# Optimization experiments

Measured on AMD Instinct MI355X. Metric: run time of the kernel, lower is better.

Reference implementation:

```python
import jax, jax.numpy as jnp
import numpy as np

B, S, D, H, F = 4, 1024, 1024, 16, 4096
DH = D // H
EPS = 1e-5


def _ln(x, g, b):
    mu = jnp.mean(x, axis=-1, keepdims=True)
    var = jnp.mean((x - mu) ** 2, axis=-1, keepdims=True)
    return (x - mu) * jax.lax.rsqrt(var + EPS) * g + b


def _mha(q_in, k_in, v_in, mask, wq, bq, wk, bk, wv, bv, wo, bo):
    b, sq, d = q_in.shape
    sk = k_in.shape[1]
    Q = (q_in @ wq + bq).reshape(b, sq, H, DH).transpose(0, 2, 1, 3)  # [B,H,Sq,dh]
    K = (k_in @ wk + bk).reshape(b, sk, H, DH).transpose(0, 2, 1, 3)
    V = (v_in @ wv + bv).reshape(b, sk, H, DH).transpose(0, 2, 1, 3)
    scores = jnp.einsum('bhqd,bhkd->bhqk', Q, K) / jnp.sqrt(jnp.asarray(DH, Q.dtype))
    if mask is not None:
        scores = jnp.where(mask[:, None] == 0, jnp.asarray(-1e9, scores.dtype), scores)
    w = jax.nn.softmax(scores, axis=-1)
    ctx = jnp.einsum('bhqk,bhkd->bhqd', w, V).transpose(0, 2, 1, 3).reshape(b, sq, d)
    return ctx @ wo + bo


def setup_inputs() -> dict:
    key = jax.random.key(0)
    ks = jax.random.split(key, 20)
    s = 0.02
    inp = {
        'x': jax.random.normal(ks[0], (B, S, D), jnp.float32),
        'src_x': jax.random.normal(ks[1], (B, S, D), jnp.float32),
        # causal self-attention mask (1 = keep), cross mask all ones
        'mask': jnp.broadcast_to(jnp.tril(jnp.ones((S, S), jnp.int32)), (B, S, S)),
        'src_mask': jnp.ones((B, S, S), jnp.int32),
        'ln1_g': jnp.ones((D,), jnp.float32), 'ln1_b': jnp.zeros((D,), jnp.float32),
        'ln2_g': jnp.ones((D,), jnp.float32), 'ln2_b': jnp.zeros((D,), jnp.float32),
        'ln3_g': jnp.ones((D,), jnp.float32), 'ln3_b': jnp.zeros((D,), jnp.float32),
    }
    names = ['sa_wq', 'sa_wk', 'sa_wv', 'sa_wo', 'ca_wq', 'ca_wk', 'ca_wv', 'ca_wo']
    for i, n in enumerate(names):
        inp[n] = jax.random.normal(ks[2 + i], (D, D), jnp.float32) * s
        inp[n.replace('w', 'b')] = jnp.zeros((D,), jnp.float32)
    inp['ff_w1'] = jax.random.normal(ks[10], (D, F), jnp.float32) * s
    inp['ff_b1'] = jnp.zeros((F,), jnp.float32)
    inp['ff_w2'] = jax.random.normal(ks[11], (F, D), jnp.float32) * s
    inp['ff_b2'] = jnp.zeros((D,), jnp.float32)
    return inp


def reference(x, mask, src_x, src_mask,
              ln1_g, ln1_b, ln2_g, ln2_b, ln3_g, ln3_b,
              sa_wq, sa_bq, sa_wk, sa_bk, sa_wv, sa_bv, sa_wo, sa_bo,
              ca_wq, ca_bq, ca_wk, ca_bk, ca_wv, ca_bv, ca_wo, ca_bo,
              ff_w1, ff_b1, ff_w2, ff_b2):
    # pre-layer-norm decoder layer (dropout = 0 / eval mode)
    h = _ln(x, ln1_g, ln1_b)
    x = x + _mha(h, h, h, mask, sa_wq, sa_bq, sa_wk, sa_bk, sa_wv, sa_bv, sa_wo, sa_bo)
    h = _ln(x, ln2_g, ln2_b)
    x = x + _mha(h, src_x, src_x, src_mask, ca_wq, ca_bq, ca_wk, ca_bk, ca_wv, ca_bv, ca_wo, ca_bo)
    h = _ln(x, ln3_g, ln3_b)
    x = x + (jax.nn.relu(h @ ff_w1 + ff_b1) @ ff_w2 + ff_b2)
    return x
```

## Files before the change

### kernel.cpp

```cpp
#include <hip/hip_runtime.h>
#include <hip/hip_bf16.h>

#define B_ 4
#define S_ 1024
#define D_ 1024
#define H_ 16
#define DH_ 64
#define F_ 4096

typedef unsigned short u16;
typedef unsigned int u32;
typedef __attribute__((ext_vector_type(8))) short bf16x8;
typedef __attribute__((ext_vector_type(4))) short bf16x4;
typedef __attribute__((ext_vector_type(4))) float f32x4;

__device__ __forceinline__ float bf2f(u16 u) {
    return __uint_as_float(((u32)u) << 16);
}
__device__ __forceinline__ u16 f2bf(float f) {
    __hip_bfloat16 h = __float2bfloat16(f);
    return *reinterpret_cast<u16*>(&h);
}

typedef __attribute__((address_space(1))) const u32 gu32;
typedef __attribute__((address_space(3))) u32 lu32;
__device__ __forceinline__ void gl_lds16(const void* g, void* l) {
    __builtin_amdgcn_global_load_lds((gu32*)g, (lu32*)l, 16, 0, 0);
}

__global__ __launch_bounds__(256) void cvt1_kernel(const float* __restrict__ s,
                                                   u16* __restrict__ d) {
    int i = (blockIdx.x * 256 + threadIdx.x) * 4;
    float4 v = *(const float4*)(s + i);
    u16 o0 = f2bf(v.x), o1 = f2bf(v.y), o2 = f2bf(v.z), o3 = f2bf(v.w);
    d[i] = o0; d[i+1] = o1; d[i+2] = o2; d[i+3] = o3;
}

__device__ __forceinline__ void trcvt_body(const float* __restrict__ src,
                                           u16* __restrict__ dst, int K, int N,
                                           int n0, int k0) {
    __shared__ u16 tile[64][65];
    int t = threadIdx.x;
    int c = t & 63, r4 = t >> 6;
#pragma unroll
    for (int i = 0; i < 16; i++) {
        int r = i * 4 + r4;
        tile[c][r] = f2bf(src[(size_t)(k0 + r) * N + n0 + c]);
    }
    __syncthreads();
#pragma unroll
    for (int i = 0; i < 16; i++) {
        int rr = i * 4 + r4;
        dst[(size_t)(n0 + rr) * K + k0 + c] = tile[rr][c];
    }
}

__global__ __launch_bounds__(256) void trcvt_kernel(const float* __restrict__ src,
                                                    u16* __restrict__ dst,
                                                    int K, int N) {
    trcvt_body(src, dst, K, N, blockIdx.x * 64, blockIdx.y * 64);
}

struct TP { const float* src[8]; u16* dst[8]; };
__global__ __launch_bounds__(256) void trcvt8_kernel(TP tp) {
    trcvt_body(tp.src[blockIdx.z], tp.dst[blockIdx.z], D_, D_,
               blockIdx.x * 64, blockIdx.y * 64);
}

__global__ __launch_bounds__(256) void mask_reduce_kernel(const int* __restrict__ mask,
                                                          unsigned char* __restrict__ bmask) {
    int t = threadIdx.x;
    int qb = blockIdx.x >> 4, kb = blockIdx.x & 15, b = blockIdx.y;
    bool all1 = true, any1 = false;
#pragma unroll
    for (int i = 0; i < 16; i++) {
        int e = t + i * 256;
        int r = e >> 6, c = e & 63;
        int v = mask[((size_t)(b * S_ + qb * 64 + r)) * S_ + kb * 64 + c];
        all1 = all1 && (v != 0);
        any1 = any1 || (v != 0);
    }
    unsigned long long ba = __ballot(all1), bn = __ballot(any1);
    __shared__ unsigned long long sa[4], sn[4];
    if ((t & 63) == 0) { sa[t >> 6] = ba; sn[t >> 6] = bn; }
    __syncthreads();
    if (t == 0) {
        bool A = ((sa[0] & sa[1] & sa[2] & sa[3]) == ~0ull);
        bool Y = ((sn[0] | sn[1] | sn[2] | sn[3]) != 0ull);
        bmask[b * 256 + blockIdx.x] = A ? 2 : (Y ? 1 : 0);
    }
}

template<bool COPY>
__global__ __launch_bounds__(256) void ln_kernel(const float* __restrict__ xin,
                                                 const float* __restrict__ g,
                                                 const float* __restrict__ bta,
                                                 float* xcur,
                                                 u16* __restrict__ hout) {
    int row = blockIdx.x;
    int t = threadIdx.x;
    size_t base = (size_t)row * D_;
    float v[4];
#pragma unroll
    for (int i = 0; i < 4; i++) v[i] = xin[base + t + i * 256];
    float s  = v[0] + v[1] + v[2] + v[3];
    float s2 = v[0]*v[0] + v[1]*v[1] + v[2]*v[2] + v[3]*v[3];
#pragma unroll
    for (int m = 1; m < 64; m <<= 1) {
        s  += __shfl_xor(s, m);
        s2 += __shfl_xor(s2, m);
    }
    __shared__ float red[8];
    int wave = t >> 6;
    if ((t & 63) == 0) { red[wave*2] = s; red[wave*2+1] = s2; }
    __syncthreads();
    float fs  = red[0] + red[2] + red[4] + red[6];
    float fs2 = red[1] + red[3] + red[5] + red[7];
    float mu  = fs * (1.0f / D_);
    float var = fs2 * (1.0f / D_) - mu * mu;
    float rs  = rsqrtf(var + 1e-5f);
#pragma unroll
    for (int i = 0; i < 4; i++) {
        int c = t + i * 256;
        float x = v[i];
        if (COPY) xcur[base + c] = x;
        hout[base + c] = f2bf((x - mu) * rs * g[c] + bta[c]);
    }
}

struct Bias3 { const float* b0; const float* b1; const float* b2; int n1; int n2; };

__device__ __forceinline__ float bias_at(const Bias3& bs, int c) {
    const float* p; int o;
    if (c < bs.n1)      { p = bs.b0; o = c; }
    else if (c < bs.n2) { p = bs.b1; o = c - bs.n1; }
    else                { p = bs.b2; o = c - bs.n2; }
    return p[o];
}

template<int BM, int BN, int OUT_MODE, bool BIAS_ROW>
__global__ __launch_bounds__(256) void gemm128_kernel(const u16* __restrict__ A,
                                                      const u16* __restrict__ Bt,
                                                      Bias3 bias,
                                                      const float* res,
                                                      void* out,
                                                      int M, int N, int K) {
    constexpr int MT = (BM == 64) ? 4 : (BN == 64 ? 2 : 4);
    constexpr int NT = (BN == 64) ? 4 : (BM == 64 ? 2 : 4);
    __shared__ u16 As[2][BM * 64];
    __shared__ u16 Bs[2][BN * 64];
    int t = threadIdx.x;
    int m0 = blockIdx.y * BM, n0 = blockIdx.x * BN;
    int w = t >> 6, lane = t & 63, quad = lane >> 4, l16 = lane & 15;
    int wm, wn;
    if (BM == 128 && BN == 128) { wm = (w >> 1) * 64; wn = (w & 1) * 64; }
    else if (BN == 64)          { wm = w * 32;        wn = 0; }
    else                        { wm = 0;             wn = w * 32; }

    f32x4 acc[MT][NT] = {};
    int sr = lane >> 3;
    int gc = ((lane & 7) ^ sr) * 8;
    int x7 = l16 & 7;
    const u16* gA = A + (size_t)m0 * K;
    const u16* gB = Bt + (size_t)n0 * K;

    auto stage = [&](int k0, int buf) {
#pragma unroll
        for (int j = w; j < BM / 8; j += 4)
            gl_lds16(gA + (size_t)(j * 8 + sr) * K + k0 + gc, &As[buf][j * 512]);
#pragma unroll
        for (int j = w; j < BN / 8; j += 4)
            gl_lds16(gB + (size_t)(j * 8 + sr) * K + k0 + gc, &Bs[buf][j * 512]);
    };

    stage(0, 0);
    int cur = 0;
    for (int k0 = 0; k0 < K; k0 += 64) {
        __syncthreads();
        if (k0 + 64 < K) stage(k0 + 64, cur ^ 1);

#pragma unroll
        for (int s = 0; s < 2; s++) {
            bf16x8 af[MT], bfr[NT];
            int cp = ((s * 4 + quad) ^ x7) * 8;
#pragma unroll
            for (int mt = 0; mt < MT; mt++)
                af[mt] = *(const bf16x8*)&As[cur][(wm + mt * 16 + l16) * 64 + cp];
#pragma unroll
            for (int nt = 0; nt < NT; nt++)
                bfr[nt] = *(const bf16x8*)&Bs[cur][(wn + nt * 16 + l16) * 64 + cp];
#pragma unroll
            for (int mt = 0; mt < MT; mt++)
#pragma unroll
                for (int nt = 0; nt < NT; nt++)
                    acc[mt][nt] = __builtin_amdgcn_mfma_f32_16x16x32_bf16(af[mt], bfr[nt], acc[mt][nt], 0, 0, 0);
        }
        cur ^= 1;
    }

#pragma unroll
    for (int nt = 0; nt < NT; nt++) {
        int col = n0 + wn + nt * 16 + l16;
        float bc = BIAS_ROW ? 0.f : bias_at(bias, col);
#pragma unroll
        for (int mt = 0; mt < MT; mt++) {
#pragma unroll
            for (int r = 0; r < 4; r++) {
                int row = m0 + wm + mt * 16 + quad * 4 + r;
                float v = acc[mt][nt][r] + (BIAS_ROW ? bias_at(bias, row) : bc);
                if (OUT_MODE == 1) v = fmaxf(v, 0.f);
                if (OUT_MODE == 2) {
                    v += res[(size_t)row * N + col];
                    ((float*)out)[(size_t)row * N + col] = v;
                } else {
                    ((u16*)out)[(size_t)row * N + col] = f2bf(v);
                }
            }
        }
    }
}

__global__ __launch_bounds__(256) void attn_kernel(const u16* __restrict__ Q, int ldq,
                                                   const u16* __restrict__ Kb, int ldk,
                                                   const u16* __restrict__ Vt,
                                                   const int* __restrict__ mask,
                                                   const unsigned char* __restrict__ bmask,
                                                   u16* __restrict__ ctx) {
    __shared__ u16 Ks[2][2][64 * 64];
    __shared__ u16 Vs[2][2][64 * 64];
    int t = threadIdx.x;
    int b = blockIdx.z, hh = blockIdx.y;
    int w = t >> 6, lane = t & 63, quad = lane >> 4, l16 = lane & 15;
    int hoff = hh * DH_;

    int qt[2] = { (int)blockIdx.x, 15 - (int)blockIdx.x };

    bf16x8 ones8;
#pragma unroll
    for (int j = 0; j < 8; j++) ones8[j] = (short)0x3F80;

    bf16x8 qf[2][2];
#pragma unroll
    for (int tt = 0; tt < 2; tt++) {
        int qrow = qt[tt] * 64 + w * 16 + l16;
#pragma unroll
        for (int kk = 0; kk < 2; kk++) {
            bf16x8 v = *(const bf16x8*)(Q + (size_t)(b * S_ + qrow) * ldq + hoff + kk * 32 + quad * 8);
#pragma unroll
            for (int j = 0; j < 8; j++)
                v[j] = (short)f2bf(bf2f((u16)v[j]) * 0.125f);
            qf[tt][kk] = v;
        }
    }

    f32x4 oacc[2][4] = {};
    f32x4 lacc[2] = {};

    unsigned nz[2], mx[2];
#pragma unroll
    for (int tt = 0; tt < 2; tt++) {
        nz[tt] = 0; mx[tt] = 0;
        for (int c = 0; c < 16; c++) {
            int v = bmask ? (int)bmask[(b * 16 + qt[tt]) * 16 + c] : 1;
            if (v)      nz[tt] |= 1u << c;
            if (v == 1) mx[tt] |= 1u << c;
        }
    }
    unsigned nzU = nz[0] | nz[1];
    unsigned remS = 0;
    for (int s = 0; s < 8; s++) if ((nzU >> (2 * s)) & 3u) remS |= 1u << s;

    int sr = lane >> 3;
    int gc = ((lane & 7) ^ sr) * 8;

    auto stage64 = [&](int c, int buf) {
        int k0 = c * 64, c64 = c & 1;
        for (int j = w; j < 8; j += 4) {
            gl_lds16(Kb + (size_t)(b * S_ + k0 + j * 8 + sr) * ldk + hoff + gc, &Ks[buf][c64][j * 512]);
            gl_lds16(Vt + (size_t)(hoff + j * 8 + sr) * (B_ * S_) + b * S_ + k0 + gc, &Vs[buf][c64][j * 512]);
        }
    };
    auto stageS = [&](int s, int buf) {
        if ((nzU >> (2 * s)) & 1u)     stage64(2 * s, buf);
        if ((nzU >> (2 * s + 1)) & 1u) stage64(2 * s + 1, buf);
    };

    int cur = 0;
    int s = remS ? __builtin_ctz(remS) : 8;
    if (s < 8) stageS(s, 0);

    while (s < 8) {
        remS &= remS - 1;
        int ns = remS ? __builtin_ctz(remS) : 8;
        __syncthreads();
        if (ns < 8) stageS(ns, cur ^ 1);

#pragma unroll
        for (int c64 = 0; c64 < 2; c64++) {
            int c = 2 * s + c64;
            if (!((nzU >> c) & 1u)) continue;
            int k0c = c * 64;
            const u16* KsT = &Ks[cur][c64][0];
            const u16* VsT = &Vs[cur][c64][0];

#pragma unroll
            for (int tt = 0; tt < 2; tt++) {
                if (!((nz[tt] >> c) & 1u)) continue;
                bool mixed = (mx[tt] >> c) & 1u;

                float p[4][4];
#pragma unroll
                for (int nt = 0; nt < 4; nt++) {
                    f32x4 sacc = {};
                    int krow = nt * 16 + l16;
#pragma unroll
                    for (int kk = 0; kk < 2; kk++) {
                        int cp = ((kk * 4 + quad) ^ (krow & 7)) * 8;
                        bf16x8 kf = *(const bf16x8*)&KsT[krow * 64 + cp];
                        sacc = __builtin_amdgcn_mfma_f32_16x16x32_bf16(kf, qf[tt][kk], sacc, 0, 0, 0);
                    }
#pragma unroll
                    for (int r = 0; r < 4; r++) {
                        float sv = sacc[r];
                        if (mixed) {
                            int qq = qt[tt] * 64 + w * 16 + l16;
                            int kc = k0c + nt * 16 + quad * 4 + r;
                            if (mask[(size_t)(b * S_ + qq) * S_ + kc] == 0) sv = -1e9f;
                        }
                        p[nt][r] = __expf(fminf(sv, 20.f));
                    }
                }

#pragma unroll
                for (int mp = 0; mp < 2; mp++) {
                    bf16x8 af;
#pragma unroll
                    for (int r = 0; r < 4; r++) {
                        af[r]     = (short)f2bf(p[2 * mp][r]);
                        af[4 + r] = (short)f2bf(p[2 * mp + 1][r]);
                    }
                    lacc[tt] = __builtin_amdgcn_mfma_f32_16x16x32_bf16(af, ones8, lacc[tt], 0, 0, 0);
#pragma unroll
                    for (int dt = 0; dt < 4; dt++) {
                        int vrow = dt * 16 + l16;
                        int ch0 = ((2 * mp) * 2 + (quad >> 1)) ^ (vrow & 7);
                        int ch1 = ((2 * mp + 1) * 2 + (quad >> 1)) ^ (vrow & 7);
                        int off = (quad & 1) * 4;
                        bf16x4 lo = *(const bf16x4*)&VsT[vrow * 64 + ch0 * 8 + off];
                        bf16x4 hi = *(const bf16x4*)&VsT[vrow * 64 + ch1 * 8 + off];
                        bf16x8 vf;
#pragma unroll
                        for (int j = 0; j < 4; j++) { vf[j] = lo[j]; vf[4 + j] = hi[j]; }
                        oacc[tt][dt] = __builtin_amdgcn_mfma_f32_16x16x32_bf16(af, vf, oacc[tt][dt], 0, 0, 0);
                    }
                }
            }
        }
        s = ns;
        cur ^= 1;
    }

#pragma unroll
    for (int tt = 0; tt < 2; tt++)
#pragma unroll
        for (int dt = 0; dt < 4; dt++)
#pragma unroll
            for (int r = 0; r < 4; r++) {
                int qq = qt[tt] * 64 + w * 16 + quad * 4 + r;
                float l = lacc[tt][r];
                float inv = l > 0.f ? 1.f / l : 0.f;
                ctx[(size_t)(b * S_ + qq) * D_ + hoff + dt * 16 + l16] = f2bf(oacc[tt][dt][r] * inv);
            }
}

extern "C" void kernel_launch(void* const* d_in, const int* in_sizes, int n_in,
                              void* d_out, int out_size, void* d_ws, size_t ws_size,
                              hipStream_t stream) {
    const float* x     = (const float*)d_in[0];
    const float* srcx  = (const float*)d_in[1];
    const int*   mask  = (const int*)d_in[2];
    const int*   smask = (const int*)d_in[3];
    const float* ln1g = (const float*)d_in[4],  *ln1b = (const float*)d_in[5];
    const float* ln2g = (const float*)d_in[6],  *ln2b = (const float*)d_in[7];
    const float* ln3g = (const float*)d_in[8],  *ln3b = (const float*)d_in[9];
    const float* sa_wq = (const float*)d_in[10], *sa_bq = (const float*)d_in[11];
    const float* sa_wk = (const float*)d_in[12], *sa_bk = (const float*)d_in[13];
    const float* sa_wv = (const float*)d_in[14], *sa_bv = (const float*)d_in[15];
    const float* sa_wo = (const float*)d_in[16], *sa_bo = (const float*)d_in[17];
    const float* ca_wq = (const float*)d_in[18], *ca_bq = (const float*)d_in[19];
    const float* ca_wk = (const float*)d_in[20], *ca_bk = (const float*)d_in[21];
    const float* ca_wv = (const float*)d_in[22], *ca_bv = (const float*)d_in[23];
    const float* ca_wo = (const float*)d_in[24], *ca_bo = (const float*)d_in[25];
    const float* ff_w1 = (const float*)d_in[26], *ff_b1 = (const float*)d_in[27];
    const float* ff_w2 = (const float*)d_in[28], *ff_b2 = (const float*)d_in[29];

    char* ws = (char*)d_ws;
    const size_t MB = 1ull << 20;
    const size_t DD = (size_t)D_ * D_;
    float* xcur = (float*)ws;
    u16* h     = (u16*)(ws + 16 * MB);
    u16* qk    = (u16*)(ws + 24 * MB);
    u16* qb    = (u16*)(ws + 24 * MB);
    u16* kbuf  = (u16*)(ws + 32 * MB);
    u16* vt    = (u16*)(ws + 40 * MB);
    u16* ctx   = (u16*)(ws + 48 * MB);
    u16* ff    = (u16*)(ws + 24 * MB);
    u16* sxb   = (u16*)(ws + 56 * MB);
    u16* wqk_s = (u16*)(ws + 64 * MB);
    u16* wv_s  = (u16*)(ws + 68 * MB);
    u16* wo_s  = (u16*)(ws + 70 * MB);
    u16* wq_c  = (u16*)(ws + 72 * MB);
    u16* wk_c  = (u16*)(ws + 74 * MB);
    u16* wv_c  = (u16*)(ws + 76 * MB);
    u16* wo_c  = (u16*)(ws + 78 * MB);
    u16* wff1  = (u16*)(ws + 80 * MB);
    u16* wff2  = (u16*)(ws + 88 * MB);
    unsigned char* bm_self = nullptr, *bm_cross = nullptr;
    if (ws_size >= 96 * MB + 8192) {
        bm_self  = (unsigned char*)(ws + ws_size - 8192);
        bm_cross = bm_self + 4096;
    }

    dim3 blk(256);

    TP tp = {{sa_wq, sa_wk, sa_wv, sa_wo, ca_wq, ca_wk, ca_wv, ca_wo},
             {wqk_s, wqk_s + DD, wv_s, wo_s, wq_c, wk_c, wv_c, wo_c}};
    trcvt8_kernel<<<dim3(16, 16, 8), blk, 0, stream>>>(tp);
    trcvt_kernel<<<dim3(F_ / 64, D_ / 64), blk, 0, stream>>>(ff_w1, wff1, D_, F_);
    trcvt_kernel<<<dim3(D_ / 64, F_ / 64), blk, 0, stream>>>(ff_w2, wff2, F_, D_);
    cvt1_kernel<<<B_ * S_ * D_ / 1024, blk, 0, stream>>>(srcx, sxb);
    if (bm_self) {
        mask_reduce_kernel<<<dim3(256, B_), blk, 0, stream>>>(mask, bm_self);
        mask_reduce_kernel<<<dim3(256, B_), blk, 0, stream>>>(smask, bm_cross);
    }

    Bias3 bqk = { sa_bq, sa_bk, sa_bk, 1024, 2048 };
    Bias3 bsv = { sa_bv, sa_bv, sa_bv, 1 << 30, 1 << 30 };
    Bias3 bso = { sa_bo, sa_bo, sa_bo, 1 << 30, 1 << 30 };
    Bias3 bcq = { ca_bq, ca_bq, ca_bq, 1 << 30, 1 << 30 };
    Bias3 bck = { ca_bk, ca_bk, ca_bk, 1 << 30, 1 << 30 };
    Bias3 bcv = { ca_bv, ca_bv, ca_bv, 1 << 30, 1 << 30 };
    Bias3 bco = { ca_bo, ca_bo, ca_bo, 1 << 30, 1 << 30 };
    Bias3 bf1 = { ff_b1, ff_b1, ff_b1, 1 << 30, 1 << 30 };
    Bias3 bf2 = { ff_b2, ff_b2, ff_b2, 1 << 30, 1 << 30 };

    ln_kernel<true><<<B_ * S_, blk, 0, stream>>>(x, ln1g, ln1b, xcur, h);
    gemm128_kernel<128,128,0,false><<<dim3(16, 32), blk, 0, stream>>>(h, wqk_s, bqk, nullptr, qk, 4096, 2048, 1024);
    gemm128_kernel<64,128,0,true><<<dim3(32, 16), blk, 0, stream>>>(wv_s, h, bsv, nullptr, vt, 1024, 4096, 1024);
    attn_kernel<<<dim3(8, H_, B_), blk, 0, stream>>>(qk, 2048, qk + 1024, 2048, vt, mask, bm_self, ctx);
    gemm128_kernel<128,64,2,false><<<dim3(16, 32), blk, 0, stream>>>(ctx, wo_s, bso, xcur, xcur, 4096, 1024, 1024);

    ln_kernel<false><<<B_ * S_, blk, 0, stream>>>(xcur, ln2g, ln2b, nullptr, h);
    gemm128_kernel<128,64,0,false><<<dim3(16, 32), blk, 0, stream>>>(h, wq_c, bcq, nullptr, qb, 4096, 1024, 1024);
    gemm128_kernel<128,64,0,false><<<dim3(16, 32), blk, 0, stream>>>(sxb, wk_c, bck, nullptr, kbuf, 4096, 1024, 1024);
    gemm128_kernel<64,128,0,true><<<dim3(32, 16), blk, 0, stream>>>(wv_c, sxb, bcv, nullptr, vt, 1024, 4096, 1024);
    attn_kernel<<<dim3(8, H_, B_), blk, 0, stream>>>(qb, 1024, kbuf, 1024, vt, smask, bm_cross, ctx);
    gemm128_kernel<128,64,2,false><<<dim3(16, 32), blk, 0, stream>>>(ctx, wo_c, bco, xcur, xcur, 4096, 1024, 1024);

    ln_kernel<false><<<B_ * S_, blk, 0, stream>>>(xcur, ln3g, ln3b, nullptr, h);
    gemm128_kernel<128,128,1,false><<<dim3(32, 32), blk, 0, stream>>>(h, wff1, bf1, nullptr, ff, 4096, 4096, 1024);
    gemm128_kernel<128,64,2,false><<<dim3(16, 32), blk, 0, stream>>>(ff, wff2, bf2, xcur, (float*)d_out, 4096, 1024, 4096);
}
```

Before: 575.2 us.

## Split-K output projections with atomics, fuse cross Q/K GEMMs, drop double buffering

Adds an atomic-accumulate output mode and runs the attention output projections and the FF2 GEMM as split-K launches that add into the residual buffer in place. The residual copy plus ff_b2 bias is moved into the preceding layernorm kernel. Cross-attention Q and K projections are merged into one dual launch. The shared GEMM body loses its LDS double buffering, so global loads no longer overlap MFMA work. The split-K launches raise block counts for the N=1024 GEMMs, at the cost of fp32 atomic traffic and nondeterministic summation order.

```diff
diff --git a/kernel.cpp b/kernel.cpp
--- a/kernel.cpp
+++ b/kernel.cpp
@@ -96,7 +96,9 @@
                                                  const float* __restrict__ g,
                                                  const float* __restrict__ bta,
                                                  float* xcur,
-                                                 u16* __restrict__ hout) {
+                                                 u16* __restrict__ hout,
+                                                 float* preout,
+                                                 const float* __restrict__ pbias) {
     int row = blockIdx.x;
     int t = threadIdx.x;
     size_t base = (size_t)row * D_;
@@ -124,6 +126,7 @@
         int c = t + i * 256;
         float x = v[i];
         if (COPY) xcur[base + c] = x;
+        if (preout) preout[base + c] = x + pbias[c];
         hout[base + c] = f2bf((x - mu) * rs * g[c] + bta[c]);
     }
 }
@@ -136,6 +139,85 @@
     else if (c < bs.n2) { p = bs.b1; o = c - bs.n1; }
     else                { p = bs.b2; o = c - bs.n2; }
     return p[o];
+}
+
+template<int BM, int BN, int OUT_MODE, bool BIAS_ROW>
+__device__ __forceinline__ void gemm_body(u16* As, u16* Bs,
+                                          const u16* __restrict__ A,
+                                          const u16* __restrict__ Bt,
+                                          Bias3 bias, const float* res, void* out,
+                                          int M, int N, int K, int kz, int zc) {
+    constexpr int MT = (BM == 64) ? 4 : (BN == 64 ? 2 : 4);
+    constexpr int NT = (BN == 64) ? 4 : (BM == 64 ? 2 : 4);
+    int t = threadIdx.x;
+    int m0 = blockIdx.y * BM, n0 = blockIdx.x * BN;
+    int w = t >> 6, lane = t & 63, quad = lane >> 4, l16 = lane & 15;
+    int wm, wn;
+    if (BM == 128 && BN == 128) { wm = (w >> 1) * 64; wn = (w & 1) * 64; }
+    else if (BN == 64)          { wm = w * 32;        wn = 0; }
+    else                        { wm = 0;             wn = w * 32; }
+
+    f32x4 acc[MT][NT] = {};
+    int sr = lane >> 3;
+    int gc = ((lane & 7) ^ sr) * 8;
+    int x7 = l16 & 7;
+    const u16* gA = A + (size_t)m0 * K;
+    const u16* gB = Bt + (size_t)n0 * K;
+
+    int Kp = K / zc, kbeg = kz * Kp, kend = kbeg + Kp;
+    for (int k0 = kbeg; k0 < kend; k0 += 64) {
+#pragma unroll
+        for (int j = w; j < BM / 8; j += 4)
+            gl_lds16(gA + (size_t)(j * 8 + sr) * K + k0 + gc, &As[j * 512]);
+#pragma unroll
+        for (int j = w; j < BN / 8; j += 4)
+            gl_lds16(gB + (size_t)(j * 8 + sr) * K + k0 + gc, &Bs[j * 512]);
+        __syncthreads();
+
+#pragma unroll
+        for (int s = 0; s < 2; s++) {
+            bf16x8 af[MT], bfr[NT];
+            int cp = ((s * 4 + quad) ^ x7) * 8;
+#pragma unroll
+            for (int mt = 0; mt < MT; mt++)
+                af[mt] = *(const bf16x8*)&As[(wm + mt * 16 + l16) * 64 + cp];
+#pragma unroll
+            for (int nt = 0; nt < NT; nt++)
+                bfr[nt] = *(const bf16x8*)&Bs[(wn + nt * 16 + l16) * 64 + cp];
+#pragma unroll
+            for (int mt = 0; mt < MT; mt++)
+#pragma unroll
+                for (int nt = 0; nt < NT; nt++)
+                    acc[mt][nt] = __builtin_amdgcn_mfma_f32_16x16x32_bf16(af[mt], bfr[nt], acc[mt][nt], 0, 0, 0);
+        }
+        __syncthreads();
+    }
+
+#pragma unroll
+    for (int nt = 0; nt < NT; nt++) {
+        int col = n0 + wn + nt * 16 + l16;
+        float bc = 0.f;
+        if (OUT_MODE == 3) { if (bias.b0 && kz == 0) bc = bias_at(bias, col); }
+        else if (!BIAS_ROW) bc = bias_at(bias, col);
+#pragma unroll
+        for (int mt = 0; mt < MT; mt++) {
+#pragma unroll
+            for (int r = 0; r < 4; r++) {
+                int row = m0 + wm + mt * 16 + quad * 4 + r;
+                float v = acc[mt][nt][r] +
+                          ((OUT_MODE != 3 && BIAS_ROW) ? bias_at(bias, row) : bc);
+                if (OUT_MODE == 1) v = fmaxf(v, 0.f);
+                if (OUT_MODE == 2) {
+                    v += res[(size_t)row * N + col];
+                    ((float*)out)[(size_t)row * N + col] = v;
+                } else if (OUT_MODE == 3) {
+                    atomicAdd(&((float*)out)[(size_t)row * N + col], v);
+                } else {
+                    ((u16*)out)[(size_t)row * N + col] = f2bf(v);
+                }
+            }
+        }
+    }
 }
 
 template<int BM, int BN, int OUT_MODE, bool BIAS_ROW>
@@ -145,79 +227,23 @@
                                                       const float* res,
                                                       void* out,
                                                       int M, int N, int K) {
-    constexpr int MT = (BM == 64) ? 4 : (BN == 64 ? 2 : 4);
-    constexpr int NT = (BN == 64) ? 4 : (BM == 64 ? 2 : 4);
-    __shared__ u16 As[2][BM * 64];
-    __shared__ u16 Bs[2][BN * 64];
-    int t = threadIdx.x;
-    int m0 = blockIdx.y * BM, n0 = blockIdx.x * BN;
-    int w = t >> 6, lane = t & 63, quad = lane >> 4, l16 = lane & 15;
-    int wm, wn;
-    if (BM == 128 && BN == 128) { wm = (w >> 1) * 64; wn = (w & 1) * 64; }
-    else if (BN == 64)          { wm = w * 32;        wn = 0; }
-    else                        { wm = 0;             wn = w * 32; }
-
-    f32x4 acc[MT][NT] = {};
-    int sr = lane >> 3;
-    int gc = ((lane & 7) ^ sr) * 8;
-    int x7 = l16 & 7;
-    const u16* gA = A + (size_t)m0 * K;
-    const u16* gB = Bt + (size_t)n0 * K;
-
-    auto stage = [&](int k0, int buf) {
-#pragma unroll
-        for (int j = w; j < BM / 8; j += 4)
-            gl_lds16(gA + (size_t)(j * 8 + sr) * K + k0 + gc, &As[buf][j * 512]);
-#pragma unroll
-        for (int j = w; j < BN / 8; j += 4)
-            gl_lds16(gB + (size_t)(j * 8 + sr) * K + k0 + gc, &Bs[buf][j * 512]);
-    };
-
-    stage(0, 0);
-    int cur = 0;
-    for (int k0 = 0; k0 < K; k0 += 64) {
-        __syncthreads();
-        if (k0 + 64 < K) stage(k0 + 64, cur ^ 1);
-
-#pragma unroll
-        for (int s = 0; s < 2; s++) {
-            bf16x8 af[MT], bfr[NT];
-            int cp = ((s * 4 + quad) ^ x7) * 8;
-#pragma unroll
-            for (int mt = 0; mt < MT; mt++)
-                af[mt] = *(const bf16x8*)&As[cur][(wm + mt * 16 + l16) * 64 + cp];
-#pragma unroll
-            for (int nt = 0; nt < NT; nt++)
-                bfr[nt] = *(const bf16x8*)&Bs[cur][(wn + nt * 16 + l16) * 64 + cp];
-#pragma unroll
-            for (int mt = 0; mt < MT; mt++)
-#pragma unroll
-                for (int nt = 0; nt < NT; nt++)
-                    acc[mt][nt] = __builtin_amdgcn_mfma_f32_16x16x32_bf16(af[mt], bfr[nt], acc[mt][nt], 0, 0, 0);
-        }
-        cur ^= 1;
-    }
-
-#pragma unroll
-    for (int nt = 0; nt < NT; nt++) {
-        int col = n0 + wn + nt * 16 + l16;
-        float bc = BIAS_ROW ? 0.f : bias_at(bias, col);
-#pragma unroll
-        for (int mt = 0; mt < MT; mt++) {
-#pragma unroll
-            for (int r = 0; r < 4; r++) {
-                int row = m0 + wm + mt * 16 + quad * 4 + r;
-                float v = acc[mt][nt][r] + (BIAS_ROW ? bias_at(bias, row) : bc);
-                if (OUT_MODE == 1) v = fmaxf(v, 0.f);
-                if (OUT_MODE == 2) {
-                    v += res[(size_t)row * N + col];
-                    ((float*)out)[(size_t)row * N + col] = v;
-                } else {
-                    ((u16*)out)[(size_t)row * N + col] = f2bf(v);
-                }
-            }
-        }
-    }
+    __shared__ u16 As[BM * 64];
+    __shared__ u16 Bs[BN * 64];
+    gemm_body<BM, BN, OUT_MODE, BIAS_ROW>(As, Bs, A, Bt, bias, res, out,
+                                          M, N, K, blockIdx.z, gridDim.z);
+}
+
+__global__ __launch_bounds__(256) void gemm_dual_kernel(const u16* A0, const u16* Bt0,
+                                                        Bias3 b0, void* o0,
+                                                        const u16* A1, const u16* Bt1,
+                                                        Bias3 b1, void* o1,
+                                                        int M, int N, int K) {
+    __shared__ u16 As[128 * 64];
+    __shared__ u16 Bs[64 * 64];
+    bool z = blockIdx.z != 0;
+    gemm_body<128, 64, 0, false>(As, Bs, z ? A1 : A0, z ? Bt1 : Bt0,
+                                 z ? b1 : b0, nullptr, z ? o1 : o0,
+                                 M, N, K, 0, 1);
 }
 
 __global__ __launch_bounds__(256) void attn_kernel(const u16* __restrict__ Q, int ldq,
@@ -442,22 +468,23 @@
     Bias3 bcv = { ca_bv, ca_bv, ca_bv, 1 << 30, 1 << 30 };
     Bias3 bco = { ca_bo, ca_bo, ca_bo, 1 << 30, 1 << 30 };
     Bias3 bf1 = { ff_b1, ff_b1, ff_b1, 1 << 30, 1 << 30 };
-    Bias3 bf2 = { ff_b2, ff_b2, ff_b2, 1 << 30, 1 << 30 };
-
-    ln_kernel<true><<<B_ * S_, blk, 0, stream>>>(x, ln1g, ln1b, xcur, h);
+    Bias3 bnul = { nullptr, nullptr, nullptr, 1 << 30, 1 << 30 };
+
+    ln_kernel<true><<<B_ * S_, blk, 0, stream>>>(x, ln1g, ln1b, xcur, h, nullptr, nullptr);
     gemm128_kernel<128,128,0,false><<<dim3(16, 32), blk, 0, stream>>>(h, wqk_s, bqk, nullptr, qk, 4096, 2048, 1024);
     gemm128_kernel<64,128,0,true><<<dim3(32, 16), blk, 0, stream>>>(wv_s, h, bsv, nullptr, vt, 1024, 4096, 1024);
     attn_kernel<<<dim3(8, H_, B_), blk, 0, stream>>>(qk, 2048, qk + 1024, 2048, vt, mask, bm_self, ctx);
-    gemm128_kernel<128,64,2,false><<<dim3(16, 32), blk, 0, stream>>>(ctx, wo_s, bso, xcur, xcur, 4096, 1024, 1024);
-
-    ln_kernel<false><<<B_ * S_, blk, 0, stream>>>(xcur, ln2g, ln2b, nullptr, h);
-    gemm128_kernel<128,64,0,false><<<dim3(16, 32), blk, 0, stream>>>(h, wq_c, bcq, nullptr, qb, 4096, 1024, 1024);
-    gemm128_kernel<128,64,0,false><<<dim3(16, 32), blk, 0, stream>>>(sxb, wk_c, bck, nullptr, kbuf, 4096, 1024, 1024);
+    gemm128_kernel<128,64,3,false><<<dim3(16, 32, 2), blk, 0, stream>>>(ctx, wo_s, bso, nullptr, xcur, 4096, 1024, 1024);
+
+    ln_kernel<false><<<B_ * S_, blk, 0, stream>>>(xcur, ln2g, ln2b, nullptr, h, nullptr, nullptr);
+    gemm_dual_kernel<<<dim3(16, 32, 2), blk, 0, stream>>>(h, wq_c, bcq, qb,
+                                                          sxb, wk_c, bck, kbuf,
+                                                          4096, 1024, 1024);
     gemm128_kernel<64,128,0,true><<<dim3(32, 16), blk, 0, stream>>>(wv_c, sxb, bcv, nullptr, vt, 1024, 4096, 1024);
     attn_kernel<<<dim3(8, H_, B_), blk, 0, stream>>>(qb, 1024, kbuf, 1024, vt, smask, bm_cross, ctx);
-    gemm128_kernel<128,64,2,false><<<dim3(16, 32), blk, 0, stream>>>(ctx, wo_c, bco, xcur, xcur, 4096, 1024, 1024);
-
-    ln_kernel<false><<<B_ * S_, blk, 0, stream>>>(xcur, ln3g, ln3b, nullptr, h);
+    gemm128_kernel<128,64,3,false><<<dim3(16, 32, 2), blk, 0, stream>>>(ctx, wo_c, bco, nullptr, xcur, 4096, 1024, 1024);
+
+    ln_kernel<false><<<B_ * S_, blk, 0, stream>>>(xcur, ln3g, ln3b, nullptr, h, (float*)d_out, ff_b2);
     gemm128_kernel<128,128,1,false><<<dim3(32, 32), blk, 0, stream>>>(h, wff1, bf1, nullptr, ff, 4096, 4096, 1024);
-    gemm128_kernel<128,64,2,false><<<dim3(16, 32), blk, 0, stream>>>(ff, wff2, bf2, xcur, (float*)d_out, 4096, 1024, 4096);
-}
+    gemm128_kernel<128,64,3,false><<<dim3(16, 32, 4), blk, 0, stream>>>(ff, wff2, bnul, nullptr, (float*)d_out, 4096, 1024, 4096);
+}
```

Result: slower. 601.2 us (+4.5%).
